# Performance work log

Hardware: AMD Instinct MI355X
Metric: run time of the kernel (lower is better)

Reference implementation:

```python
import jax, jax.numpy as jnp
import numpy as np

RADIUS = 2
ITERATION = 8
KSIZE = 2 * RADIUS + 1


def _side_window_kernels():
    """Build the 8 directional box kernels exactly as in the torch module.
    Returns (8, 1, k, k) float32: order L, R, U, D, NW, NE, SW, SE."""
    r, k = RADIUS, KSIZE
    ones = np.ones((k, k), np.float32)
    L = ones.copy(); L[:, r + 1:] = 0
    R = ones.copy(); R[:, :r] = 0
    U = ones.copy(); U[r + 1:, :] = 0
    D = ones.copy(); D[:r, :] = 0
    # diagonal kernels are cloned from U/D BEFORE normalization (as in source)
    NW, NE, SW, SE = U.copy(), U.copy(), D.copy(), D.copy()
    n_half = (r + 1) * k
    L, R, U, D = L / n_half, R / n_half, U / n_half, D / n_half
    NW[:, r + 1:] = 0; NE[:, :r] = 0; SW[:, r + 1:] = 0; SE[:, :r] = 0
    n_quad = float((r + 1) ** 2)
    NW, NE, SW, SE = NW / n_quad, NE / n_quad, SW / n_quad, SE / n_quad
    return np.stack([L, R, U, D, NW, NE, SW, SE])[:, None]  # (8,1,k,k)


def setup_inputs() -> dict:
    key = jax.random.key(0)
    # HWC image with pixel values in [0, 255)
    img = jax.random.uniform(key, (2048, 2048, 3), dtype=jnp.float32) * 255.0
    return {"img": img}


def reference(img) -> jnp.ndarray:
    kern = jnp.asarray(_side_window_kernels())          # (8,1,k,k)
    x0 = jnp.transpose(img, (2, 0, 1))[:, None]          # (C,1,H,W): channels as batch

    def step(im, _):
        # replicate padding, then valid conv with all 8 directional kernels at once
        p = jnp.pad(im, ((0, 0), (0, 0), (RADIUS, RADIUS), (RADIUS, RADIUS)), mode="edge")
        conv = jax.lax.conv_general_dilated(p, kern, (1, 1), "VALID")  # (C,8,H,W)
        d = conv - im                                    # broadcast (C,1,H,W)->(C,8,H,W)
        idx = jnp.argmin(jnp.abs(d), axis=1, keepdims=True)
        dm = jnp.take_along_axis(d, idx, axis=1)         # (C,1,H,W)
        return im + dm, None

    res, _ = jax.lax.scan(step, x0, None, length=ITERATION)
    diff = jnp.abs(x0 - res)[:, 0]                       # (C,H,W)
    out = jnp.transpose(diff, (1, 2, 0))                 # (H,W,C)
    return jnp.clip(out, 0.0, 255.0)
```

## Files before the change

kernel.cpp:

```cpp
#include <hip/hip_runtime.h>


static constexpr int H  = 2048;
static constexpr int W  = 2048;
static constexpr int C  = 3;
static constexpr int WC = W * C;

__device__ __forceinline__ void apply_phase_r(float* __restrict__ a,
                                              const float* __restrict__ r,
                                              int k, int ph, float& center,
                                              float w15, float w9) {
  const float t0 = r[k+2], t1 = r[k+5], t2 = r[k+8],
              t3 = r[k+11], t4 = r[k+14];
  if (ph == 2) center = t2;
  a[0]=__builtin_fmaf(w15,t0,a[0]); a[0]=__builtin_fmaf(w15,t1,a[0]); a[0]=__builtin_fmaf(w15,t2,a[0]);
  a[1]=__builtin_fmaf(w15,t2,a[1]); a[1]=__builtin_fmaf(w15,t3,a[1]); a[1]=__builtin_fmaf(w15,t4,a[1]);
  if (ph <= 2) {
    a[2]=__builtin_fmaf(w15,t0,a[2]); a[2]=__builtin_fmaf(w15,t1,a[2]); a[2]=__builtin_fmaf(w15,t2,a[2]);
    a[2]=__builtin_fmaf(w15,t3,a[2]); a[2]=__builtin_fmaf(w15,t4,a[2]);
    a[4]=__builtin_fmaf(w9,t0,a[4]); a[4]=__builtin_fmaf(w9,t1,a[4]); a[4]=__builtin_fmaf(w9,t2,a[4]);
    a[5]=__builtin_fmaf(w9,t2,a[5]); a[5]=__builtin_fmaf(w9,t3,a[5]); a[5]=__builtin_fmaf(w9,t4,a[5]);
  }
  if (ph >= 2) {
    a[3]=__builtin_fmaf(w15,t0,a[3]); a[3]=__builtin_fmaf(w15,t1,a[3]); a[3]=__builtin_fmaf(w15,t2,a[3]);
    a[3]=__builtin_fmaf(w15,t3,a[3]); a[3]=__builtin_fmaf(w15,t4,a[3]);
    a[6]=__builtin_fmaf(w9,t0,a[6]); a[6]=__builtin_fmaf(w9,t1,a[6]); a[6]=__builtin_fmaf(w9,t2,a[6]);
    a[7]=__builtin_fmaf(w9,t2,a[7]); a[7]=__builtin_fmaf(w9,t3,a[7]); a[7]=__builtin_fmaf(w9,t4,a[7]);
  }
}

__device__ __forceinline__ float finish(const float* __restrict__ a,
                                        float center) {
  float best  = a[0] - center;
  float besta = fabsf(best);
#pragma unroll
  for (int m = 1; m < 8; ++m) {
    const float d  = a[m] - center;
    const float ab = fabsf(d);
    if (ab < besta) { besta = ab; best = d; }
  }
  return center + best;
}

template<bool FINAL>
__global__
__attribute__((amdgpu_flat_work_group_size(256, 256), amdgpu_waves_per_eu(2, 3)))
void swf_pg(const float* __restrict__ src, float* __restrict__ dst,
            const float* __restrict__ x0) {
  const int col4 = (blockIdx.x * 256 + threadIdx.x) * 4;
  const int yA   = blockIdx.y * 2;

  const float w15 = 1.0f / 15.0f;
  const float w9  = 1.0f / 9.0f;

  float accA[4][8], accB[4][8];
#pragma unroll
  for (int k = 0; k < 4; ++k)
#pragma unroll
    for (int m = 0; m < 8; ++m) { accA[k][m] = 0.0f; accB[k][m] = 0.0f; }
  float centerA[4], centerB[4];

  const bool fastc = (col4 >= 8) && (col4 <= WC - 12);
  if (fastc) {
    const float* colbase = src + (col4 - 8);
#pragma unroll
    for (int i = 0; i < 6; ++i) {
      int hy = yA + i - 2;
      hy = hy < 0 ? 0 : (hy > H - 1 ? H - 1 : hy);
      const float4* rp = (const float4*)(colbase + (size_t)hy * WC);
      const float4 q0 = rp[0], q1 = rp[1], q2 = rp[2], q3 = rp[3], q4 = rp[4];
      const float r[20] = {q0.x,q0.y,q0.z,q0.w, q1.x,q1.y,q1.z,q1.w,
                           q2.x,q2.y,q2.z,q2.w, q3.x,q3.y,q3.z,q3.w,
                           q4.x,q4.y,q4.z,q4.w};
#pragma unroll
      for (int k = 0; k < 4; ++k) {
        if (i <= 4) apply_phase_r(accA[k], r, k, i,     centerA[k], w15, w9);
        if (i >= 1) apply_phase_r(accB[k], r, k, i - 1, centerB[k], w15, w9);
      }
    }
  } else {
    const int base = col4 - 8;
#pragma unroll
    for (int i = 0; i < 6; ++i) {
      int hy = yA + i - 2;
      hy = hy < 0 ? 0 : (hy > H - 1 ? H - 1 : hy);
      const float* rr = src + (size_t)hy * WC;
      float r[20];
#pragma unroll
      for (int x = 0; x < 20; ++x) {
        const int f = base + x;
        const int idx = (f < 0)    ? ((f % 3) + 3) % 3
                      : (f >= WC)  ? (W - 1) * 3 + (f % 3)
                      : f;
        r[x] = rr[idx];
      }
#pragma unroll
      for (int k = 0; k < 4; ++k) {
        if (i <= 4) apply_phase_r(accA[k], r, k, i,     centerA[k], w15, w9);
        if (i >= 1) apply_phase_r(accB[k], r, k, i - 1, centerB[k], w15, w9);
      }
    }
  }

#pragma unroll
  for (int half = 0; half < 2; ++half) {
    const int y = yA + half;
    float4 xv4;
    if (FINAL) xv4 = *(const float4*)(x0 + (size_t)y * WC + col4);
    float o[4];
#pragma unroll
    for (int k = 0; k < 4; ++k) {
      const float res = half ? finish(accB[k], centerB[k])
                             : finish(accA[k], centerA[k]);
      if (FINAL) {
        const float xv = (k == 0) ? xv4.x : (k == 1) ? xv4.y
                       : (k == 2) ? xv4.z : xv4.w;
        float diff = fabsf(xv - res);
        o[k] = diff > 255.0f ? 255.0f : diff;
      } else {
        o[k] = res;
      }
    }
    float4 ov;
    ov.x = o[0]; ov.y = o[1]; ov.z = o[2]; ov.w = o[3];
    *(float4*)(dst + (size_t)y * WC + col4) = ov;
  }
}

extern "C" void kernel_launch(void* const* d_in, const int* in_sizes, int n_in,
                              void* d_out, int out_size, void* d_ws, size_t ws_size,
                              hipStream_t stream) {
  const float* x0  = (const float*)d_in[0];
  float*       out = (float*)d_out;
  float*       ws  = (float*)d_ws;

  dim3 grid(WC / 1024, H / 2);
  dim3 block(256);

  swf_pg<false><<<grid, block, 0, stream>>>(x0,  ws,  nullptr);
  swf_pg<false><<<grid, block, 0, stream>>>(ws,  out, nullptr);
  swf_pg<false><<<grid, block, 0, stream>>>(out, ws,  nullptr);
  swf_pg<false><<<grid, block, 0, stream>>>(ws,  out, nullptr);
  swf_pg<false><<<grid, block, 0, stream>>>(out, ws,  nullptr);
  swf_pg<false><<<grid, block, 0, stream>>>(ws,  out, nullptr);
  swf_pg<false><<<grid, block, 0, stream>>>(out, ws,  nullptr);
  swf_pg<true ><<<grid, block, 0, stream>>>(ws,  out, x0);
}
```

Baseline: 531.9 us.

## Remap blocks to XCD-local row bands and emit first row early to cut registers

Workgroup IDs are remapped so that each of the 8 XCDs processes a contiguous band of row pairs, which improves L2 reuse of the overlapping halo rows between neighbouring blocks. The first output row is written right after its five input rows are accumulated, so its accumulators die before the sixth row is loaded, which lowers register pressure. The waves_per_eu hint is raised to 4 to allow higher occupancy. The risks are spills if the register budget is too tight, and the remap assumes round-robin dispatch of blocks across XCDs.

Result: slower. 544.4 us (+2.4%).

```diff
diff --git a/kernel.cpp b/kernel.cpp
--- a/kernel.cpp
+++ b/kernel.cpp
@@ -1,10 +1,14 @@
 #include <hip/hip_runtime.h>
 
 
-static constexpr int H  = 2048;
-static constexpr int W  = 2048;
-static constexpr int C  = 3;
-static constexpr int WC = W * C;
+static constexpr int H      = 2048;
+static constexpr int W      = 2048;
+static constexpr int C      = 3;
+static constexpr int WC     = W * C;
+static constexpr int NBX    = 6;
+static constexpr int NPAIRS = H / 2;
+static constexpr int NWG    = NBX * NPAIRS;
+static constexpr int BAND   = NPAIRS / 8;
 
 __device__ __forceinline__ void apply_phase_r(float* __restrict__ a,
                                               const float* __restrict__ r,
@@ -43,12 +47,44 @@
 }
 
 template<bool FINAL>
+__device__ __forceinline__ void emit_row(const float acc[4][8],
+                                         const float* __restrict__ center,
+                                         int y, int col4,
+                                         const float* __restrict__ x0,
+                                         float* __restrict__ dst) {
+  float4 xv4;
+  if (FINAL) xv4 = *(const float4*)(x0 + (size_t)y * WC + col4);
+  float o[4];
+#pragma unroll
+  for (int k = 0; k < 4; ++k) {
+    const float res = finish(acc[k], center[k]);
+    if (FINAL) {
+      const float xv = (k == 0) ? xv4.x : (k == 1) ? xv4.y
+                     : (k == 2) ? xv4.z : xv4.w;
+      float diff = fabsf(xv - res);
+      o[k] = diff > 255.0f ? 255.0f : diff;
+    } else {
+      o[k] = res;
+    }
+  }
+  float4 ov;
+  ov.x = o[0]; ov.y = o[1]; ov.z = o[2]; ov.w = o[3];
+  *(float4*)(dst + (size_t)y * WC + col4) = ov;
+}
+
+template<bool FINAL>
 __global__
-__attribute__((amdgpu_flat_work_group_size(256, 256), amdgpu_waves_per_eu(2, 3)))
+__attribute__((amdgpu_flat_work_group_size(256, 256), amdgpu_waves_per_eu(4)))
 void swf_pg(const float* __restrict__ src, float* __restrict__ dst,
             const float* __restrict__ x0) {
-  const int col4 = (blockIdx.x * 256 + threadIdx.x) * 4;
-  const int yA   = blockIdx.y * 2;
+  const int flat  = blockIdx.y * NBX + blockIdx.x;
+  const int xcd   = flat & 7;
+  const int idx   = flat >> 3;
+  const int yb    = idx / NBX;
+  const int xb    = idx - yb * NBX;
+  const int ypair = xcd * BAND + yb;
+  const int col4  = (xb * 256 + threadIdx.x) * 4;
+  const int yA    = ypair * 2;
 
   const float w15 = 1.0f / 15.0f;
   const float w9  = 1.0f / 9.0f;
@@ -64,7 +100,7 @@
   if (fastc) {
     const float* colbase = src + (col4 - 8);
 #pragma unroll
-    for (int i = 0; i < 6; ++i) {
+    for (int i = 0; i < 5; ++i) {
       int hy = yA + i - 2;
       hy = hy < 0 ? 0 : (hy > H - 1 ? H - 1 : hy);
       const float4* rp = (const float4*)(colbase + (size_t)hy * WC);
@@ -74,14 +110,28 @@
                            q4.x,q4.y,q4.z,q4.w};
 #pragma unroll
       for (int k = 0; k < 4; ++k) {
-        if (i <= 4) apply_phase_r(accA[k], r, k, i,     centerA[k], w15, w9);
+        apply_phase_r(accA[k], r, k, i, centerA[k], w15, w9);
         if (i >= 1) apply_phase_r(accB[k], r, k, i - 1, centerB[k], w15, w9);
       }
     }
+    emit_row<FINAL>(accA, centerA, yA, col4, x0, dst);
+    {
+      int hy = yA + 3;
+      hy = hy > H - 1 ? H - 1 : hy;
+      const float4* rp = (const float4*)(colbase + (size_t)hy * WC);
+      const float4 q0 = rp[0], q1 = rp[1], q2 = rp[2], q3 = rp[3], q4 = rp[4];
+      const float r[20] = {q0.x,q0.y,q0.z,q0.w, q1.x,q1.y,q1.z,q1.w,
+                           q2.x,q2.y,q2.z,q2.w, q3.x,q3.y,q3.z,q3.w,
+                           q4.x,q4.y,q4.z,q4.w};
+#pragma unroll
+      for (int k = 0; k < 4; ++k)
+        apply_phase_r(accB[k], r, k, 4, centerB[k], w15, w9);
+    }
+    emit_row<FINAL>(accB, centerB, yA + 1, col4, x0, dst);
   } else {
     const int base = col4 - 8;
 #pragma unroll
-    for (int i = 0; i < 6; ++i) {
+    for (int i = 0; i < 5; ++i) {
       int hy = yA + i - 2;
       hy = hy < 0 ? 0 : (hy > H - 1 ? H - 1 : hy);
       const float* rr = src + (size_t)hy * WC;
@@ -89,41 +139,36 @@
 #pragma unroll
       for (int x = 0; x < 20; ++x) {
         const int f = base + x;
-        const int idx = (f < 0)    ? ((f % 3) + 3) % 3
-                      : (f >= WC)  ? (W - 1) * 3 + (f % 3)
-                      : f;
-        r[x] = rr[idx];
+        const int idx2 = (f < 0)    ? ((f % 3) + 3) % 3
+                       : (f >= WC)  ? (W - 1) * 3 + (f % 3)
+                       : f;
+        r[x] = rr[idx2];
       }
 #pragma unroll
       for (int k = 0; k < 4; ++k) {
-        if (i <= 4) apply_phase_r(accA[k], r, k, i,     centerA[k], w15, w9);
+        apply_phase_r(accA[k], r, k, i, centerA[k], w15, w9);
         if (i >= 1) apply_phase_r(accB[k], r, k, i - 1, centerB[k], w15, w9);
       }
     }
-  }
-
+    emit_row<FINAL>(accA, centerA, yA, col4, x0, dst);
+    {
+      int hy = yA + 3;
+      hy = hy > H - 1 ? H - 1 : hy;
+      const float* rr = src + (size_t)hy * WC;
+      float r[20];
 #pragma unroll
-  for (int half = 0; half < 2; ++half) {
-    const int y = yA + half;
-    float4 xv4;
-    if (FINAL) xv4 = *(const float4*)(x0 + (size_t)y * WC + col4);
-    float o[4];
+      for (int x = 0; x < 20; ++x) {
+        const int f = base + x;
+        const int idx2 = (f < 0)    ? ((f % 3) + 3) % 3
+                       : (f >= WC)  ? (W - 1) * 3 + (f % 3)
+                       : f;
+        r[x] = rr[idx2];
+      }
 #pragma unroll
-    for (int k = 0; k < 4; ++k) {
-      const float res = half ? finish(accB[k], centerB[k])
-                             : finish(accA[k], centerA[k]);
-      if (FINAL) {
-        const float xv = (k == 0) ? xv4.x : (k == 1) ? xv4.y
-                       : (k == 2) ? xv4.z : xv4.w;
-        float diff = fabsf(xv - res);
-        o[k] = diff > 255.0f ? 255.0f : diff;
-      } else {
-        o[k] = res;
-      }
+      for (int k = 0; k < 4; ++k)
+        apply_phase_r(accB[k], r, k, 4, centerB[k], w15, w9);
     }
-    float4 ov;
-    ov.x = o[0]; ov.y = o[1]; ov.z = o[2]; ov.w = o[3];
-    *(float4*)(dst + (size_t)y * WC + col4) = ov;
+    emit_row<FINAL>(accB, centerB, yA + 1, col4, x0, dst);
   }
 }
 
@@ -134,7 +179,7 @@
   float*       out = (float*)d_out;
   float*       ws  = (float*)d_ws;
 
-  dim3 grid(WC / 1024, H / 2);
+  dim3 grid(NBX, NPAIRS);
   dim3 block(256);
 
   swf_pg<false><<<grid, block, 0, stream>>>(x0,  ws,  nullptr);
```

## Use packed FMA, XCD-aware row-band block remap, and raise occupancy target

Applied to the files above, without the earlier changes.

Accumulators are reorganized into 2-wide float vectors so the stencil sums use packed FMA (v_pk_fma_f32), halving the FMA instruction count. Block indices are remapped so each of the 8 XCDs processes a contiguous band of row pairs, improving L2 reuse of halo rows across neighbouring blocks. The waves-per-EU hint changes from 2-3 to 4, which may constrain registers and cause spills in exchange for higher occupancy.

New measurement: 669.5 us. +25.9%, slower.

```diff
diff --git a/kernel.cpp b/kernel.cpp
--- a/kernel.cpp
+++ b/kernel.cpp
@@ -1,41 +1,54 @@
 #include <hip/hip_runtime.h>
 
 
-static constexpr int H  = 2048;
-static constexpr int W  = 2048;
-static constexpr int C  = 3;
-static constexpr int WC = W * C;
+static constexpr int H      = 2048;
+static constexpr int W      = 2048;
+static constexpr int C      = 3;
+static constexpr int WC     = W * C;
+static constexpr int NBX    = 6;
+static constexpr int NPAIRS = H / 2;
+static constexpr int BAND   = NPAIRS / 8;
 
-__device__ __forceinline__ void apply_phase_r(float* __restrict__ a,
-                                              const float* __restrict__ r,
-                                              int k, int ph, float& center,
-                                              float w15, float w9) {
-  const float t0 = r[k+2], t1 = r[k+5], t2 = r[k+8],
-              t3 = r[k+11], t4 = r[k+14];
+typedef float v2f __attribute__((ext_vector_type(2)));
+
+__device__ __forceinline__ v2f pkfma(v2f a, v2f b, v2f c) {
+  return __builtin_elementwise_fma(a, b, c);
+}
+
+__device__ __forceinline__ void apply_phase_pk(v2f* __restrict__ a,
+                                               const float* __restrict__ r,
+                                               int kp, int ph, v2f& center,
+                                               v2f w15, v2f w9) {
+  const int b = 2 * kp;
+  const v2f t0 = {r[b+2],  r[b+3]};
+  const v2f t1 = {r[b+5],  r[b+6]};
+  const v2f t2 = {r[b+8],  r[b+9]};
+  const v2f t3 = {r[b+11], r[b+12]};
+  const v2f t4 = {r[b+14], r[b+15]};
   if (ph == 2) center = t2;
-  a[0]=__builtin_fmaf(w15,t0,a[0]); a[0]=__builtin_fmaf(w15,t1,a[0]); a[0]=__builtin_fmaf(w15,t2,a[0]);
-  a[1]=__builtin_fmaf(w15,t2,a[1]); a[1]=__builtin_fmaf(w15,t3,a[1]); a[1]=__builtin_fmaf(w15,t4,a[1]);
+  a[0]=pkfma(w15,t0,a[0]); a[0]=pkfma(w15,t1,a[0]); a[0]=pkfma(w15,t2,a[0]);
+  a[1]=pkfma(w15,t2,a[1]); a[1]=pkfma(w15,t3,a[1]); a[1]=pkfma(w15,t4,a[1]);
   if (ph <= 2) {
-    a[2]=__builtin_fmaf(w15,t0,a[2]); a[2]=__builtin_fmaf(w15,t1,a[2]); a[2]=__builtin_fmaf(w15,t2,a[2]);
-    a[2]=__builtin_fmaf(w15,t3,a[2]); a[2]=__builtin_fmaf(w15,t4,a[2]);
-    a[4]=__builtin_fmaf(w9,t0,a[4]); a[4]=__builtin_fmaf(w9,t1,a[4]); a[4]=__builtin_fmaf(w9,t2,a[4]);
-    a[5]=__builtin_fmaf(w9,t2,a[5]); a[5]=__builtin_fmaf(w9,t3,a[5]); a[5]=__builtin_fmaf(w9,t4,a[5]);
+    a[2]=pkfma(w15,t0,a[2]); a[2]=pkfma(w15,t1,a[2]); a[2]=pkfma(w15,t2,a[2]);
+    a[2]=pkfma(w15,t3,a[2]); a[2]=pkfma(w15,t4,a[2]);
+    a[4]=pkfma(w9,t0,a[4]); a[4]=pkfma(w9,t1,a[4]); a[4]=pkfma(w9,t2,a[4]);
+    a[5]=pkfma(w9,t2,a[5]); a[5]=pkfma(w9,t3,a[5]); a[5]=pkfma(w9,t4,a[5]);
   }
   if (ph >= 2) {
-    a[3]=__builtin_fmaf(w15,t0,a[3]); a[3]=__builtin_fmaf(w15,t1,a[3]); a[3]=__builtin_fmaf(w15,t2,a[3]);
-    a[3]=__builtin_fmaf(w15,t3,a[3]); a[3]=__builtin_fmaf(w15,t4,a[3]);
-    a[6]=__builtin_fmaf(w9,t0,a[6]); a[6]=__builtin_fmaf(w9,t1,a[6]); a[6]=__builtin_fmaf(w9,t2,a[6]);
-    a[7]=__builtin_fmaf(w9,t2,a[7]); a[7]=__builtin_fmaf(w9,t3,a[7]); a[7]=__builtin_fmaf(w9,t4,a[7]);
+    a[3]=pkfma(w15,t0,a[3]); a[3]=pkfma(w15,t1,a[3]); a[3]=pkfma(w15,t2,a[3]);
+    a[3]=pkfma(w15,t3,a[3]); a[3]=pkfma(w15,t4,a[3]);
+    a[6]=pkfma(w9,t0,a[6]); a[6]=pkfma(w9,t1,a[6]); a[6]=pkfma(w9,t2,a[6]);
+    a[7]=pkfma(w9,t2,a[7]); a[7]=pkfma(w9,t3,a[7]); a[7]=pkfma(w9,t4,a[7]);
   }
 }
 
-__device__ __forceinline__ float finish(const float* __restrict__ a,
-                                        float center) {
-  float best  = a[0] - center;
+__device__ __forceinline__ float finish_half(const v2f* __restrict__ a,
+                                             float center, int h) {
+  float best  = a[0][h] - center;
   float besta = fabsf(best);
 #pragma unroll
   for (int m = 1; m < 8; ++m) {
-    const float d  = a[m] - center;
+    const float d  = a[m][h] - center;
     const float ab = fabsf(d);
     if (ab < besta) { besta = ab; best = d; }
   }
@@ -43,22 +56,60 @@
 }
 
 template<bool FINAL>
+__device__ __forceinline__ void emit_row(const v2f acc[2][8],
+                                         const v2f* __restrict__ center,
+                                         int y, int col4,
+                                         const float* __restrict__ x0,
+                                         float* __restrict__ dst) {
+  float4 xv4;
+  if (FINAL) xv4 = *(const float4*)(x0 + (size_t)y * WC + col4);
+  float o[4];
+#pragma unroll
+  for (int kp = 0; kp < 2; ++kp)
+#pragma unroll
+    for (int h = 0; h < 2; ++h) {
+      const int k = 2 * kp + h;
+      const float res = finish_half(acc[kp], center[kp][h], h);
+      if (FINAL) {
+        const float xv = (k == 0) ? xv4.x : (k == 1) ? xv4.y
+                       : (k == 2) ? xv4.z : xv4.w;
+        float diff = fabsf(xv - res);
+        o[k] = diff > 255.0f ? 255.0f : diff;
+      } else {
+        o[k] = res;
+      }
+    }
+  float4 ov;
+  ov.x = o[0]; ov.y = o[1]; ov.z = o[2]; ov.w = o[3];
+  *(float4*)(dst + (size_t)y * WC + col4) = ov;
+}
+
+template<bool FINAL>
 __global__
-__attribute__((amdgpu_flat_work_group_size(256, 256), amdgpu_waves_per_eu(2, 3)))
-void swf_pg(const float* __restrict__ src, float* __restrict__ dst,
+__attribute__((amdgpu_flat_work_group_size(256, 256), amdgpu_waves_per_eu(4, 4)))
+void swf_pk(const float* __restrict__ src, float* __restrict__ dst,
             const float* __restrict__ x0) {
-  const int col4 = (blockIdx.x * 256 + threadIdx.x) * 4;
-  const int yA   = blockIdx.y * 2;
+  const int flat  = blockIdx.y * NBX + blockIdx.x;
+  const int xcd   = flat & 7;
+  const int idx   = flat >> 3;
+  const int yb    = idx / NBX;
+  const int xb    = idx - yb * NBX;
+  const int ypair = xcd * BAND + yb;
+  const int col4  = (xb * 256 + threadIdx.x) * 4;
+  const int yA    = ypair * 2;
 
-  const float w15 = 1.0f / 15.0f;
-  const float w9  = 1.0f / 9.0f;
+  const v2f w15 = {1.0f / 15.0f, 1.0f / 15.0f};
+  const v2f w9  = {1.0f / 9.0f,  1.0f / 9.0f};
 
-  float accA[4][8], accB[4][8];
+  v2f accA[2][8], accB[2][8];
 #pragma unroll
-  for (int k = 0; k < 4; ++k)
+  for (int kp = 0; kp < 2; ++kp)
 #pragma unroll
-    for (int m = 0; m < 8; ++m) { accA[k][m] = 0.0f; accB[k][m] = 0.0f; }
-  float centerA[4], centerB[4];
+    for (int m = 0; m < 8; ++m) {
+      accA[kp][m] = (v2f){0.0f, 0.0f};
+      accB[kp][m] = (v2f){0.0f, 0.0f};
+    }
+  v2f centerA[2], centerB[2];
 
   const bool fastc = (col4 >= 8) && (col4 <= WC - 12);
   if (fastc) {
@@ -73,9 +124,9 @@
                            q2.x,q2.y,q2.z,q2.w, q3.x,q3.y,q3.z,q3.w,
                            q4.x,q4.y,q4.z,q4.w};
 #pragma unroll
-      for (int k = 0; k < 4; ++k) {
-        if (i <= 4) apply_phase_r(accA[k], r, k, i,     centerA[k], w15, w9);
-        if (i >= 1) apply_phase_r(accB[k], r, k, i - 1, centerB[k], w15, w9);
+      for (int kp = 0; kp < 2; ++kp) {
+        if (i <= 4) apply_phase_pk(accA[kp], r, kp, i,     centerA[kp], w15, w9);
+        if (i >= 1) apply_phase_pk(accB[kp], r, kp, i - 1, centerB[kp], w15, w9);
       }
     }
   } else {
@@ -89,42 +140,21 @@
 #pragma unroll
       for (int x = 0; x < 20; ++x) {
         const int f = base + x;
-        const int idx = (f < 0)    ? ((f % 3) + 3) % 3
-                      : (f >= WC)  ? (W - 1) * 3 + (f % 3)
-                      : f;
-        r[x] = rr[idx];
+        const int ix = (f < 0)    ? ((f % 3) + 3) % 3
+                     : (f >= WC)  ? (W - 1) * 3 + (f % 3)
+                     : f;
+        r[x] = rr[ix];
       }
 #pragma unroll
-      for (int k = 0; k < 4; ++k) {
-        if (i <= 4) apply_phase_r(accA[k], r, k, i,     centerA[k], w15, w9);
-        if (i >= 1) apply_phase_r(accB[k], r, k, i - 1, centerB[k], w15, w9);
+      for (int kp = 0; kp < 2; ++kp) {
+        if (i <= 4) apply_phase_pk(accA[kp], r, kp, i,     centerA[kp], w15, w9);
+        if (i >= 1) apply_phase_pk(accB[kp], r, kp, i - 1, centerB[kp], w15, w9);
       }
     }
   }
 
-#pragma unroll
-  for (int half = 0; half < 2; ++half) {
-    const int y = yA + half;
-    float4 xv4;
-    if (FINAL) xv4 = *(const float4*)(x0 + (size_t)y * WC + col4);
-    float o[4];
-#pragma unroll
-    for (int k = 0; k < 4; ++k) {
-      const float res = half ? finish(accB[k], centerB[k])
-                             : finish(accA[k], centerA[k]);
-      if (FINAL) {
-        const float xv = (k == 0) ? xv4.x : (k == 1) ? xv4.y
-                       : (k == 2) ? xv4.z : xv4.w;
-        float diff = fabsf(xv - res);
-        o[k] = diff > 255.0f ? 255.0f : diff;
-      } else {
-        o[k] = res;
-      }
-    }
-    float4 ov;
-    ov.x = o[0]; ov.y = o[1]; ov.z = o[2]; ov.w = o[3];
-    *(float4*)(dst + (size_t)y * WC + col4) = ov;
-  }
+  emit_row<FINAL>(accA, centerA, yA,     col4, x0, dst);
+  emit_row<FINAL>(accB, centerB, yA + 1, col4, x0, dst);
 }
 
 extern "C" void kernel_launch(void* const* d_in, const int* in_sizes, int n_in,
@@ -134,15 +164,15 @@
   float*       out = (float*)d_out;
   float*       ws  = (float*)d_ws;
 
-  dim3 grid(WC / 1024, H / 2);
+  dim3 grid(NBX, NPAIRS);
   dim3 block(256);
 
-  swf_pg<false><<<grid, block, 0, stream>>>(x0,  ws,  nullptr);
-  swf_pg<false><<<grid, block, 0, stream>>>(ws,  out, nullptr);
-  swf_pg<false><<<grid, block, 0, stream>>>(out, ws,  nullptr);
-  swf_pg<false><<<grid, block, 0, stream>>>(ws,  out, nullptr);
-  swf_pg<false><<<grid, block, 0, stream>>>(out, ws,  nullptr);
-  swf_pg<false><<<grid, block, 0, stream>>>(ws,  out, nullptr);
-  swf_pg<false><<<grid, block, 0, stream>>>(out, ws,  nullptr);
-  swf_pg<true ><<<grid, block, 0, stream>>>(ws,  out, x0);
+  swf_pk<false><<<grid, block, 0, stream>>>(x0,  ws,  nullptr);
+  swf_pk<false><<<grid, block, 0, stream>>>(ws,  out, nullptr);
+  swf_pk<false><<<grid, block, 0, stream>>>(out, ws,  nullptr);
+  swf_pk<false><<<grid, block, 0, stream>>>(ws,  out, nullptr);
+  swf_pk<false><<<grid, block, 0, stream>>>(out, ws,  nullptr);
+  swf_pk<false><<<grid, block, 0, stream>>>(ws,  out, nullptr);
+  swf_pk<false><<<grid, block, 0, stream>>>(out, ws,  nullptr);
+  swf_pk<true ><<<grid, block, 0, stream>>>(ws,  out, x0);
 }
```

## Compute one row per thread with XCD-aware band block mapping and row prefetch

Applied to the files above, without the earlier changes.

Each thread now produces one output row instead of two, which drops the shared 6-row window reuse and halves accumulator registers. Blocks are remapped so that each of the 8 XCDs handles a contiguous horizontal band of rows, aiming for better L2 locality of the overlapping halo rows. Source rows are software-prefetched one step ahead, and occupancy is pinned at 3 waves per EU. The trade-off is more global and cache loads per output (5 rows per output row instead of 3).

New measurement: 686.4 us. +29.0%, slower.

```diff
diff --git a/kernel.cpp b/kernel.cpp
--- a/kernel.cpp
+++ b/kernel.cpp
@@ -1,17 +1,18 @@
 #include <hip/hip_runtime.h>
 
 
-static constexpr int H  = 2048;
-static constexpr int W  = 2048;
-static constexpr int C  = 3;
-static constexpr int WC = W * C;
+static constexpr int H    = 2048;
+static constexpr int W    = 2048;
+static constexpr int C    = 3;
+static constexpr int WC   = W * C;
+static constexpr int NBX  = 6;
+static constexpr int BAND = H / 8;
 
-__device__ __forceinline__ void apply_phase_r(float* __restrict__ a,
-                                              const float* __restrict__ r,
-                                              int k, int ph, float& center,
+__device__ __forceinline__ void apply_phase_t(float* __restrict__ a,
+                                              float t0, float t1, float t2,
+                                              float t3, float t4,
+                                              int ph, float& center,
                                               float w15, float w9) {
-  const float t0 = r[k+2], t1 = r[k+5], t2 = r[k+8],
-              t3 = r[k+11], t4 = r[k+14];
   if (ph == 2) center = t2;
   a[0]=__builtin_fmaf(w15,t0,a[0]); a[0]=__builtin_fmaf(w15,t1,a[0]); a[0]=__builtin_fmaf(w15,t2,a[0]);
   a[1]=__builtin_fmaf(w15,t2,a[1]); a[1]=__builtin_fmaf(w15,t3,a[1]); a[1]=__builtin_fmaf(w15,t4,a[1]);
@@ -43,88 +44,99 @@
 }
 
 template<bool FINAL>
-__global__
-__attribute__((amdgpu_flat_work_group_size(256, 256), amdgpu_waves_per_eu(2, 3)))
-void swf_pg(const float* __restrict__ src, float* __restrict__ dst,
+__global__ __attribute__((amdgpu_waves_per_eu(3, 3))) __launch_bounds__(256)
+void swf_sr(const float* __restrict__ src, float* __restrict__ dst,
             const float* __restrict__ x0) {
-  const int col4 = (blockIdx.x * 256 + threadIdx.x) * 4;
-  const int yA   = blockIdx.y * 2;
+  const int flat = blockIdx.y * NBX + blockIdx.x;
+  const int xcd  = flat & 7;
+  const int idx  = flat >> 3;
+  const int yb   = idx / NBX;
+  const int xb   = idx - yb * NBX;
+  const int y    = xcd * BAND + yb;
+  const int col4 = (xb * 256 + threadIdx.x) * 4;
 
   const float w15 = 1.0f / 15.0f;
   const float w9  = 1.0f / 9.0f;
 
-  float accA[4][8], accB[4][8];
+  float acc[4][8];
 #pragma unroll
   for (int k = 0; k < 4; ++k)
 #pragma unroll
-    for (int m = 0; m < 8; ++m) { accA[k][m] = 0.0f; accB[k][m] = 0.0f; }
-  float centerA[4], centerB[4];
+    for (int m = 0; m < 8; ++m) acc[k][m] = 0.0f;
+  float center[4];
 
   const bool fastc = (col4 >= 8) && (col4 <= WC - 12);
   if (fastc) {
     const float* colbase = src + (col4 - 8);
+
+    int hy0 = y - 2;
+    hy0 = hy0 < 0 ? 0 : hy0;
+    const float4* rp0 = (const float4*)(colbase + (size_t)hy0 * WC);
+    float4 q0 = rp0[0], q1 = rp0[1], q2 = rp0[2], q3 = rp0[3], q4 = rp0[4];
+
 #pragma unroll
-    for (int i = 0; i < 6; ++i) {
-      int hy = yA + i - 2;
-      hy = hy < 0 ? 0 : (hy > H - 1 ? H - 1 : hy);
-      const float4* rp = (const float4*)(colbase + (size_t)hy * WC);
-      const float4 q0 = rp[0], q1 = rp[1], q2 = rp[2], q3 = rp[3], q4 = rp[4];
+    for (int j = 0; j < 5; ++j) {
+      float4 p0, p1, p2, p3, p4;
+      if (j < 4) {
+        int hy = y + (j + 1) - 2;
+        hy = hy < 0 ? 0 : (hy > H - 1 ? H - 1 : hy);
+        const float4* rp = (const float4*)(colbase + (size_t)hy * WC);
+        p0 = rp[0]; p1 = rp[1]; p2 = rp[2]; p3 = rp[3]; p4 = rp[4];
+      }
       const float r[20] = {q0.x,q0.y,q0.z,q0.w, q1.x,q1.y,q1.z,q1.w,
                            q2.x,q2.y,q2.z,q2.w, q3.x,q3.y,q3.z,q3.w,
                            q4.x,q4.y,q4.z,q4.w};
 #pragma unroll
       for (int k = 0; k < 4; ++k) {
-        if (i <= 4) apply_phase_r(accA[k], r, k, i,     centerA[k], w15, w9);
-        if (i >= 1) apply_phase_r(accB[k], r, k, i - 1, centerB[k], w15, w9);
+        const float t0 = r[k+2], t1 = r[k+5], t2 = r[k+8],
+                    t3 = r[k+11], t4 = r[k+14];
+        apply_phase_t(acc[k], t0,t1,t2,t3,t4, j, center[k], w15, w9);
       }
+      if (j < 4) { q0 = p0; q1 = p1; q2 = p2; q3 = p3; q4 = p4; }
     }
   } else {
     const int base = col4 - 8;
 #pragma unroll
-    for (int i = 0; i < 6; ++i) {
-      int hy = yA + i - 2;
+    for (int j = 0; j < 5; ++j) {
+      int hy = y + j - 2;
       hy = hy < 0 ? 0 : (hy > H - 1 ? H - 1 : hy);
       const float* rr = src + (size_t)hy * WC;
       float r[20];
 #pragma unroll
       for (int x = 0; x < 20; ++x) {
-        const int f = base + x;
-        const int idx = (f < 0)    ? ((f % 3) + 3) % 3
-                      : (f >= WC)  ? (W - 1) * 3 + (f % 3)
-                      : f;
-        r[x] = rr[idx];
+        const int f  = base + x;
+        const int ix = (f < 0)    ? ((f % 3) + 3) % 3
+                     : (f >= WC)  ? (W - 1) * 3 + (f % 3)
+                     : f;
+        r[x] = rr[ix];
       }
 #pragma unroll
       for (int k = 0; k < 4; ++k) {
-        if (i <= 4) apply_phase_r(accA[k], r, k, i,     centerA[k], w15, w9);
-        if (i >= 1) apply_phase_r(accB[k], r, k, i - 1, centerB[k], w15, w9);
+        const float t0 = r[k+2], t1 = r[k+5], t2 = r[k+8],
+                    t3 = r[k+11], t4 = r[k+14];
+        apply_phase_t(acc[k], t0,t1,t2,t3,t4, j, center[k], w15, w9);
       }
     }
   }
 
+  float4 xv4;
+  if (FINAL) xv4 = *(const float4*)(x0 + (size_t)y * WC + col4);
+  float o[4];
 #pragma unroll
-  for (int half = 0; half < 2; ++half) {
-    const int y = yA + half;
-    float4 xv4;
-    if (FINAL) xv4 = *(const float4*)(x0 + (size_t)y * WC + col4);
-    float o[4];
-#pragma unroll
-    for (int k = 0; k < 4; ++k) {
-      const float res = half ? finish(accB[k], centerB[k])
-                             : finish(accA[k], centerA[k]);
-      if (FINAL) {
-        const float xv = (k == 0) ? xv4.x : (k == 1) ? xv4.y
-                       : (k == 2) ? xv4.z : xv4.w;
-        float diff = fabsf(xv - res);
-        o[k] = diff > 255.0f ? 255.0f : diff;
-      } else {
-        o[k] = res;
-      }
+  for (int k = 0; k < 4; ++k) {
+    const float res = finish(acc[k], center[k]);
+    if (FINAL) {
+      const float xv = (k == 0) ? xv4.x : (k == 1) ? xv4.y
+                     : (k == 2) ? xv4.z : xv4.w;
+      float diff = fabsf(xv - res);
+      o[k] = diff > 255.0f ? 255.0f : diff;
+    } else {
+      o[k] = res;
     }
-    float4 ov;
-    ov.x = o[0]; ov.y = o[1]; ov.z = o[2]; ov.w = o[3];
-    *(float4*)(dst + (size_t)y * WC + col4) = ov;
   }
+  float4 ov;
+  ov.x = o[0]; ov.y = o[1]; ov.z = o[2]; ov.w = o[3];
+  *(float4*)(dst + (size_t)y * WC + col4) = ov;
 }
 
 extern "C" void kernel_launch(void* const* d_in, const int* in_sizes, int n_in,
@@ -134,15 +146,15 @@
   float*       out = (float*)d_out;
   float*       ws  = (float*)d_ws;
 
-  dim3 grid(WC / 1024, H / 2);
+  dim3 grid(NBX, H);
   dim3 block(256);
 
-  swf_pg<false><<<grid, block, 0, stream>>>(x0,  ws,  nullptr);
-  swf_pg<false><<<grid, block, 0, stream>>>(ws,  out, nullptr);
-  swf_pg<false><<<grid, block, 0, stream>>>(out, ws,  nullptr);
-  swf_pg<false><<<grid, block, 0, stream>>>(ws,  out, nullptr);
-  swf_pg<false><<<grid, block, 0, stream>>>(out, ws,  nullptr);
-  swf_pg<false><<<grid, block, 0, stream>>>(ws,  out, nullptr);
-  swf_pg<false><<<grid, block, 0, stream>>>(out, ws,  nullptr);
-  swf_pg<true ><<<grid, block, 0, stream>>>(ws,  out, x0);
+  swf_sr<false><<<grid, block, 0, stream>>>(x0,  ws,  nullptr);
+  swf_sr<false><<<grid, block, 0, stream>>>(ws,  out, nullptr);
+  swf_sr<false><<<grid, block, 0, stream>>>(out, ws,  nullptr);
+  swf_sr<false><<<grid, block, 0, stream>>>(ws,  out, nullptr);
+  swf_sr<false><<<grid, block, 0, stream>>>(out, ws,  nullptr);
+  swf_sr<false><<<grid, block, 0, stream>>>(ws,  out, nullptr);
+  swf_sr<false><<<grid, block, 0, stream>>>(out, ws,  nullptr);
+  swf_sr<true ><<<grid, block, 0, stream>>>(ws,  out, x0);
 }
```
